# Kernel tuning notes

Measured on AMD Instinct MI355X. Metric: run time of the kernel, lower is better.

## Reference

```python
import jax, jax.numpy as jnp
import numpy as np


def setup_inputs() -> dict:
    key = jax.random.key(0)
    ks = jax.random.split(key, 8)
    B, C, S = 32, 64, 64          # batch, per-atom channels, molecule size
    CC = 128                      # x_concat channels; CC + 2*C == OC
    OC = 256                      # conv block channels
    w = lambda k, shp: jax.random.normal(k, shp, dtype=jnp.float32) * 0.05
    return {
        "x": jax.random.normal(ks[0], (B, C, S), dtype=jnp.float32),
        "xc": jax.random.normal(ks[1], (B, CC, S - 1, S), dtype=jnp.float32),
        "W1": w(ks[2], (OC, OC)), "b1": w(ks[3], (OC,)),
        "W2": w(ks[4], (OC, OC)), "b2": w(ks[5], (OC,)),
        "W3": w(ks[6], (OC, OC)), "b3": w(ks[7], (OC,)),
        "batch_size": B,
        "size": S,
    }


def _conv1x1_relu(h, W, b):
    # 1x1 Conv2d == per-position matmul over channels
    return jax.nn.relu(jnp.einsum('bchw,oc->bohw', h, W) + b[None, :, None, None])


def reference(x, xc, W1, b1, W2, b2, W3, b3, batch_size, size):
    # Build pair matrix: for shift d+1, roll[d, i] = (i - (d+1)) % size
    i = jnp.arange(size)
    d = jnp.arange(1, size)
    idx = (i[None, :] - d[:, None]) % size            # [S-1, S]
    rolled = x[:, :, idx]                              # [B, C, S-1, S] gather
    x_rep = jnp.broadcast_to(x[:, :, None, :], rolled.shape)
    # torch.cat((*x_concat, pair_matrix), dim=1): concat channels then [x_rep, rolled]
    pairs_cat = jnp.concatenate([xc, x_rep, rolled], axis=1)  # [B, OC, S-1, S]
    h = _conv1x1_relu(pairs_cat, W1, b1)
    h = _conv1x1_relu(h, W2, b2)
    h = _conv1x1_relu(h, W3, b3)
    return h
```

## Files before the change

### kernel.cpp

```cpp
#include <hip/hip_runtime.h>
#include <stdint.h>


typedef __attribute__((ext_vector_type(8))) __bf16 bf16x8;
typedef __attribute__((ext_vector_type(4))) float f32x4;
typedef __attribute__((ext_vector_type(4))) unsigned short u16x4;
typedef __attribute__((ext_vector_type(8))) unsigned short u16x8;

__device__ __forceinline__ unsigned short f2bf(float f) {
  unsigned int u = __builtin_bit_cast(unsigned int, f);
  u += 0x7FFFu + ((u >> 16) & 1u);
  return (unsigned short)(u >> 16);
}

__device__ __forceinline__ int xaddr(int pos, int c) {
  int slot = (pos << 5) + (c >> 3);
  slot ^= (pos & 7);
  return (slot << 3) + (c & 7);
}

__global__ void wconv_kernel(const float* __restrict__ W1, const float* __restrict__ W2,
                             const float* __restrict__ W3, unsigned short* __restrict__ wb) {
  int i = (blockIdx.x * 256 + threadIdx.x) * 4;
  const float* Ws[3] = {W1, W2, W3};
#pragma unroll
  for (int L = 0; L < 3; ++L) {
    f32x4 a = *(const f32x4*)(Ws[L] + i);
    u16x4 p;
#pragma unroll
    for (int v = 0; v < 4; ++v) p[v] = f2bf(a[v]);
    *(u16x4*)(wb + L * 65536 + i) = p;
  }
}

__global__ __launch_bounds__(512, 2)
void fused_kernel(const float* __restrict__ x, const float* __restrict__ xc,
                  const unsigned short* __restrict__ wb,
                  const float* __restrict__ b1, const float* __restrict__ b2,
                  const float* __restrict__ b3, float* __restrict__ out) {
  __shared__ __align__(16) unsigned char lraw[73728];
  unsigned short* X   = (unsigned short*)lraw;
  unsigned short* stg = (unsigned short*)(lraw + 65536);
  float* bounce = (float*)lraw;

  const int r = blockIdx.x;
  const int b0 = r / 63;
  const int dd = r % 63;
  const int d = dd + 1;
  const int tid = threadIdx.x;
  const int lane = tid & 63;
  const int g16 = lane >> 4;
  const int l16 = lane & 15;
  const int wv = tid >> 6;

  auto ldrnd = [&](int rd, f32x4 ld[2]) {
    int rr = rd / 3;
    int ck = rd - rr * 3;
    int b = b0 + 16 * rr;
#pragma unroll
    for (int it = 0; it < 2; ++it) {
      int u = it * 512 + tid, cc = u >> 4, i4 = (u & 15) << 2;
      const float* src = (ck < 2)
          ? xc + (((b * 128 + ck * 64 + cc) * 63) + dd) * 64 + i4
          : x + (b * 64 + cc) * 64 + i4;
      ld[it] = *(const f32x4*)src;
    }
  };

  f32x4 ld[2];
  ldrnd(0, ld);
  for (int rd = 0; rd < 6; ++rd) {
    int rr = rd / 3;
    int ck = rd - rr * 3;
#pragma unroll
    for (int it = 0; it < 2; ++it) {
      int u = it * 512 + tid, cc = u >> 4, i4 = (u & 15) << 2;
      u16x4 p;
#pragma unroll
      for (int v = 0; v < 4; ++v) p[v] = f2bf(ld[it][v]);
      *(u16x4*)&stg[cc * 64 + i4] = p;
    }
    if (rd < 5) ldrnd(rd + 1, ld);
    __syncthreads();
    int nsub = (ck == 2) ? 2 : 1;
    for (int sub = 0; sub < nsub; ++sub) {
      int cbase = (ck + sub) * 64;
      int i = tid & 63;
      int c0 = (tid >> 6) << 3;
      int ieff = (sub == 1) ? ((i - d + 64) & 63) : i;
      u16x8 p;
#pragma unroll
      for (int j = 0; j < 8; ++j) p[j] = stg[(c0 + j) * 64 + ieff];
      *(u16x8*)&X[xaddr(rr * 64 + i, cbase + c0)] = p;
    }
    __syncthreads();
  }

  for (int layer = 0; layer < 3; ++layer) {
    const unsigned short* wl = wb + layer * 65536;
    const float* bias = (layer == 0) ? b1 : (layer == 1) ? b2 : b3;

    f32x4 acc[2][8] = {};
    const int ow = wv * 32;

#pragma unroll 2
    for (int kk = 0; kk < 8; ++kk) {
      int kb = kk * 32 + g16 * 8;
      bf16x8 afr[2];
#pragma unroll
      for (int mf = 0; mf < 2; ++mf)
        afr[mf] = __builtin_bit_cast(
            bf16x8, *(const u16x8*)(wl + (ow + mf * 16 + l16) * 256 + kb));
      bf16x8 bfr[4];
#pragma unroll
      for (int nf = 0; nf < 4; ++nf)
        bfr[nf] = __builtin_bit_cast(bf16x8, *(const u16x8*)&X[xaddr(nf * 16 + l16, kb)]);
#pragma unroll
      for (int mf = 0; mf < 2; ++mf)
#pragma unroll
        for (int nf = 0; nf < 4; ++nf)
          acc[mf][nf] = __builtin_amdgcn_mfma_f32_16x16x32_bf16(afr[mf], bfr[nf], acc[mf][nf], 0, 0, 0);
#pragma unroll
      for (int nf = 0; nf < 4; ++nf)
        bfr[nf] = __builtin_bit_cast(bf16x8, *(const u16x8*)&X[xaddr(64 + nf * 16 + l16, kb)]);
#pragma unroll
      for (int mf = 0; mf < 2; ++mf)
#pragma unroll
        for (int nf = 0; nf < 4; ++nf)
          acc[mf][4 + nf] = __builtin_amdgcn_mfma_f32_16x16x32_bf16(afr[mf], bfr[nf], acc[mf][4 + nf], 0, 0, 0);
    }
    __syncthreads();

    if (layer < 2) {
#pragma unroll
      for (int mf = 0; mf < 2; ++mf) {
        int o0 = ow + mf * 16 + g16 * 4;
        f32x4 bv = *(const f32x4*)(bias + o0);
#pragma unroll
        for (int nf = 0; nf < 8; ++nf) {
          int pos = nf * 16 + l16;
          u16x4 p;
#pragma unroll
          for (int v = 0; v < 4; ++v)
            p[v] = f2bf(fmaxf(acc[mf][nf][v] + bv[v], 0.f));
          *(u16x4*)&X[xaddr(pos, o0)] = p;
        }
      }
      __syncthreads();
    } else {
      bool first = true;
#pragma unroll
      for (int rr = 0; rr < 2; ++rr) {
#pragma unroll
        for (int h = 0; h < 2; ++h) {
          if (!first) __syncthreads();
          first = false;
          if ((wv >> 2) == h) {
#pragma unroll
            for (int mf = 0; mf < 2; ++mf) {
              int olb = (wv & 3) * 32 + mf * 16 + g16 * 4;
              f32x4 bv = *(const f32x4*)(bias + h * 128 + olb);
#pragma unroll
              for (int nq = 0; nq < 4; ++nq) {
                int pos = nq * 16 + l16;
#pragma unroll
                for (int v = 0; v < 4; ++v) {
                  int ol = olb + v;
                  bounce[ol * 64 + (pos ^ ((ol & 7) << 2))] =
                      fmaxf(acc[mf][rr * 4 + nq][v] + bv[v], 0.f);
                }
              }
            }
          }
          __syncthreads();
          int bq = b0 + 16 * rr;
#pragma unroll
          for (int q = 0; q < 4; ++q) {
            int u = q * 512 + tid;
            int oh = u >> 4;
            int pos4 = (u & 15) << 2;
            f32x4 vv = *(const f32x4*)&bounce[oh * 64 + (pos4 ^ ((oh & 7) << 2))];
            int o = h * 128 + oh;
            *(f32x4*)&out[(((bq * 256 + o) * 63) + dd) * 64 + pos4] = vv;
          }
        }
      }
    }
  }
}

extern "C" void kernel_launch(void* const* d_in, const int* in_sizes, int n_in,
                              void* d_out, int out_size, void* d_ws, size_t ws_size,
                              hipStream_t stream) {
  const float* x  = (const float*)d_in[0];
  const float* xc = (const float*)d_in[1];
  const float* W1 = (const float*)d_in[2];
  const float* b1 = (const float*)d_in[3];
  const float* W2 = (const float*)d_in[4];
  const float* b2 = (const float*)d_in[5];
  const float* W3 = (const float*)d_in[6];
  const float* b3 = (const float*)d_in[7];
  float* out = (float*)d_out;
  unsigned short* wb = (unsigned short*)d_ws;

  wconv_kernel<<<64, 256, 0, stream>>>(W1, W2, W3, wb);
  fused_kernel<<<1008, 512, 0, stream>>>(x, xc, wb, b1, b2, b3, out);
}
```

Baseline: 110.4 us.

## Read rolled pair channels via shifted LDS index and double-buffer staging

```diff
diff --git a/kernel.cpp b/kernel.cpp
--- a/kernel.cpp
+++ b/kernel.cpp
@@ -14,9 +14,8 @@
 }
 
 __device__ __forceinline__ int xaddr(int pos, int c) {
-  int slot = (pos << 5) + (c >> 3);
-  slot ^= (pos & 7);
-  return (slot << 3) + (c & 7);
+  int slot = (pos << 3) + ((((c & 63) >> 3) ^ pos) & 7);
+  return ((c >> 6) << 13) + (slot << 3) + (c & 7);
 }
 
 __global__ void wconv_kernel(const float* __restrict__ W1, const float* __restrict__ W2,
@@ -33,15 +32,16 @@
   }
 }
 
-__global__ __launch_bounds__(512, 2)
+__global__ __launch_bounds__(512, 4)
 void fused_kernel(const float* __restrict__ x, const float* __restrict__ xc,
                   const unsigned short* __restrict__ wb,
                   const float* __restrict__ b1, const float* __restrict__ b2,
                   const float* __restrict__ b3, float* __restrict__ out) {
-  __shared__ __align__(16) unsigned char lraw[73728];
-  unsigned short* X   = (unsigned short*)lraw;
-  unsigned short* stg = (unsigned short*)(lraw + 65536);
+  __shared__ __align__(16) unsigned char lraw[65536];
+  unsigned short* X = (unsigned short*)lraw;
   float* bounce = (float*)lraw;
+  unsigned short* stg0 = (unsigned short*)(lraw + 49152);
+  unsigned short* stg1 = (unsigned short*)(lraw + 57344);
 
   const int r = blockIdx.x;
   const int b0 = r / 63;
@@ -70,35 +70,34 @@
   f32x4 ld[2];
   ldrnd(0, ld);
   for (int rd = 0; rd < 6; ++rd) {
-    int rr = rd / 3;
-    int ck = rd - rr * 3;
+    unsigned short* sb = (rd & 1) ? stg1 : stg0;
 #pragma unroll
     for (int it = 0; it < 2; ++it) {
       int u = it * 512 + tid, cc = u >> 4, i4 = (u & 15) << 2;
       u16x4 p;
 #pragma unroll
       for (int v = 0; v < 4; ++v) p[v] = f2bf(ld[it][v]);
-      *(u16x4*)&stg[cc * 64 + i4] = p;
+      *(u16x4*)&sb[cc * 64 + i4] = p;
     }
     if (rd < 5) ldrnd(rd + 1, ld);
     __syncthreads();
-    int nsub = (ck == 2) ? 2 : 1;
-    for (int sub = 0; sub < nsub; ++sub) {
-      int cbase = (ck + sub) * 64;
+    {
+      int rr = rd / 3;
+      int ck = rd - rr * 3;
       int i = tid & 63;
       int c0 = (tid >> 6) << 3;
-      int ieff = (sub == 1) ? ((i - d + 64) & 63) : i;
       u16x8 p;
 #pragma unroll
-      for (int j = 0; j < 8; ++j) p[j] = stg[(c0 + j) * 64 + ieff];
-      *(u16x8*)&X[xaddr(rr * 64 + i, cbase + c0)] = p;
-    }
-    __syncthreads();
+      for (int j = 0; j < 8; ++j) p[j] = sb[(c0 + j) * 64 + i];
+      *(u16x8*)&X[xaddr(rr * 64 + i, ck * 64 + c0)] = p;
+    }
   }
+  __syncthreads();
 
   for (int layer = 0; layer < 3; ++layer) {
     const unsigned short* wl = wb + layer * 65536;
     const float* bias = (layer == 0) ? b1 : (layer == 1) ? b2 : b3;
+    const bool al3 = (layer == 0);
 
     f32x4 acc[2][8] = {};
     const int ow = wv * 32;
@@ -106,6 +105,8 @@
 #pragma unroll 2
     for (int kk = 0; kk < 8; ++kk) {
       int kb = kk * 32 + g16 * 8;
+      bool a3 = al3 && (kk >= 6);
+      int cc = a3 ? (128 + (kb & 63)) : kb;
       bf16x8 afr[2];
 #pragma unroll
       for (int mf = 0; mf < 2; ++mf)
@@ -113,16 +114,22 @@
             bf16x8, *(const u16x8*)(wl + (ow + mf * 16 + l16) * 256 + kb));
       bf16x8 bfr[4];
 #pragma unroll
-      for (int nf = 0; nf < 4; ++nf)
-        bfr[nf] = __builtin_bit_cast(bf16x8, *(const u16x8*)&X[xaddr(nf * 16 + l16, kb)]);
+      for (int nf = 0; nf < 4; ++nf) {
+        int i = nf * 16 + l16;
+        int ie = a3 ? ((i - d) & 63) : i;
+        bfr[nf] = __builtin_bit_cast(bf16x8, *(const u16x8*)&X[xaddr(ie, cc)]);
+      }
 #pragma unroll
       for (int mf = 0; mf < 2; ++mf)
 #pragma unroll
         for (int nf = 0; nf < 4; ++nf)
           acc[mf][nf] = __builtin_amdgcn_mfma_f32_16x16x32_bf16(afr[mf], bfr[nf], acc[mf][nf], 0, 0, 0);
 #pragma unroll
-      for (int nf = 0; nf < 4; ++nf)
-        bfr[nf] = __builtin_bit_cast(bf16x8, *(const u16x8*)&X[xaddr(64 + nf * 16 + l16, kb)]);
+      for (int nf = 0; nf < 4; ++nf) {
+        int i = nf * 16 + l16;
+        int ie = 64 + (a3 ? ((i - d) & 63) : i);
+        bfr[nf] = __builtin_bit_cast(bf16x8, *(const u16x8*)&X[xaddr(ie, cc)]);
+      }
 #pragma unroll
       for (int mf = 0; mf < 2; ++mf)
 #pragma unroll
```

Result: slower. 165.5 us (+50.0%).
